# Performance work log

Measured on AMD Instinct MI355X. Metric: run time of the kernel, lower is better.

Reference implementation:

```python
import jax, jax.numpy as jnp
import numpy as np

B, C1, C2, H, W = 16, 64, 64, 160, 160
K, KS, HID = 4, 3, 16  # K kernels, 3x3, hidden = max(int(64/16),16)=16
EPS = 1e-5


def setup_inputs() -> dict:
    key = jax.random.key(0)
    ks = jax.random.split(key, 8)
    fan_out = KS * KS * C2
    return {
        "x": jax.random.normal(ks[0], (B, C1, H, W), jnp.float32),
        # K candidate conv kernels and biases
        "Wk": jax.random.normal(ks[1], (K, C2, C1, KS, KS), jnp.float32) * np.sqrt(2.0 / fan_out),
        "bk": jnp.zeros((K, C2), jnp.float32),
        # attention trunk: 1x1 conv C1->HID (no bias), BN, ReLU
        "Wfc": jax.random.normal(ks[2], (HID, C1), jnp.float32) * 0.1,
        "gamma_h": jnp.ones((HID,), jnp.float32),
        "beta_h": jnp.zeros((HID,), jnp.float32),
        # four attention heads
        "Wf": jax.random.normal(ks[3], (C2, HID), jnp.float32) * 0.1,
        "bf": jnp.zeros((C2,), jnp.float32),
        "Ws": jax.random.normal(ks[4], (KS * KS, HID), jnp.float32) * 0.1,
        "bs": jnp.zeros((KS * KS,), jnp.float32),
        "Wc": jax.random.normal(ks[5], (C1, HID), jnp.float32) * 0.1,
        "bc": jnp.zeros((C1,), jnp.float32),
        "Ww": jax.random.normal(ks[6], (K, HID), jnp.float32) * 0.1,
        "bw": jnp.zeros((K,), jnp.float32),
        # outer BatchNorm2d params
        "gamma_o": jnp.ones((C2,), jnp.float32),
        "beta_o": jnp.zeros((C2,), jnp.float32),
    }


def reference(x, Wk, bk, Wfc, gamma_h, beta_h, Wf, bf, Ws, bs, Wc, bc, Ww, bw, gamma_o, beta_o):
    # ---- per-sample attention over K kernels ----
    ctx = x.mean(axis=(2, 3))                      # (B, C1)  global avg pool
    h = ctx @ Wfc.T                                # (B, HID) 1x1 conv == linear
    mu = h.mean(axis=0)
    var = h.var(axis=0)                            # biased, as torch BN training
    h = (h - mu) / jnp.sqrt(var + EPS) * gamma_h + beta_h
    h = jax.nn.relu(h)
    attn_f = jax.nn.sigmoid(h @ Wf.T + bf)         # (B, C2)
    attn_s = jax.nn.sigmoid(h @ Ws.T + bs).reshape(B, KS, KS)
    attn_c = jax.nn.sigmoid(h @ Wc.T + bc)         # (B, C1)
    attn_w = jax.nn.softmax(h @ Ww.T + bw, axis=-1)  # (B, K)

    # attn: (B, K, C2, C1, KS, KS) via broadcasting
    attn = (attn_w[:, :, None, None, None, None]
            * attn_f[:, None, :, None, None, None]
            * attn_c[:, None, None, :, None, None]
            * attn_s[:, None, None, None, :, :])
    weight = jnp.sum(attn * Wk[None], axis=1)      # (B, C2, C1, KS, KS)
    bias = attn_w @ bk                             # (B, C2)

    # ---- batched conv as grouped conv with groups=B ----
    out = jax.lax.conv_general_dilated(
        x.reshape(1, B * C1, H, W),
        weight.reshape(B * C2, C1, KS, KS),
        window_strides=(1, 1), padding=((1, 1), (1, 1)),
        dimension_numbers=('NCHW', 'OIHW', 'NCHW'),
        feature_group_count=B)                     # (1, B*C2, H, W)
    out = out.reshape(B, C2, H, W) + bias[:, :, None, None]

    # ---- outer BatchNorm2d (training stats) + SiLU ----
    mu_o = out.mean(axis=(0, 2, 3))
    var_o = out.var(axis=(0, 2, 3))
    out = (out - mu_o[None, :, None, None]) / jnp.sqrt(var_o + EPS)[None, :, None, None]
    out = out * gamma_o[None, :, None, None] + beta_o[None, :, None, None]
    return out * jax.nn.sigmoid(out)               # SiLU
```

## Files before the change

kernel.cpp:

```cpp
#include <hip/hip_runtime.h>
#include <math.h>

#define BB 16
#define C1 64
#define C2 64
#define HH 160
#define WW 160
#define KK 4
#define HID 16
#define EPS 1e-5f
#define HWSZ (HH*WW)
#define NPB (BB*HWSZ)

#define WS_AF    1024
#define WS_AC    2048
#define WS_AS    3072
#define WS_AW    3216
#define WS_BIAS  3280
#define WS_STATS 4432
#define NSLOT    32
#define WS_PART  8704
#define WS_WEFF  53760
#define WS_XBF   348672
#define WS_OBF   13455872
#define WS_NEED_BYTES 106252288ULL

typedef __attribute__((ext_vector_type(8)))  short bf16x8;
typedef __attribute__((ext_vector_type(16))) float f32x16;

__device__ __forceinline__ unsigned short f2bf(float f) {
    unsigned int u = __float_as_uint(f);
    unsigned int r = (u + 0x7FFFu + ((u >> 16) & 1u)) >> 16;
    return (unsigned short)r;
}

__device__ __forceinline__ void gload16(const void* g, void* l) {
    __builtin_amdgcn_global_load_lds(
        (const __attribute__((address_space(1))) unsigned int*)g,
        (__attribute__((address_space(3))) unsigned int*)l, 16, 0, 0);
}

__global__ __launch_bounds__(256) void xprep_kernel(const float* __restrict__ x,
                                                    float* __restrict__ ws) {
    __shared__ float lds[10240];
    int bcc = blockIdx.y;
    int rg = blockIdx.x;
    int t = threadIdx.x;

    const float* src = x + (size_t)bcc * 16 * HWSZ + (size_t)rg * 4 * WW;
    float4* l4 = (float4*)lds;
    #pragma unroll
    for (int i = 0; i < 10; ++i) {
        int g = i * 256 + t;
        int ch = g / 160, rem = g - ch * 160;
        l4[g] = *(const float4*)(src + (size_t)ch * HWSZ + rem * 4);
    }
    __syncthreads();

    {
        int ch = t >> 4, j = t & 15;
        float s = 0.f;
        #pragma unroll
        for (int m = 0; m < 40; ++m) s += lds[ch * 640 + j + 16 * m];
        #pragma unroll
        for (int o = 8; o > 0; o >>= 1) s += __shfl_down(s, o, 16);
        if (j == 0) ws[WS_PART + ((size_t)bcc * 40 + rg) * 16 + ch] = s;
    }

    uint4* dst = (uint4*)(ws + WS_XBF) + ((size_t)bcc * 160 + rg * 4) * 320;
    #pragma unroll
    for (int i = 0; i < 5; ++i) {
        int u = i * 256 + t;
        int row = u / 320, rem = u - row * 320;
        int col = rem >> 1, p = rem & 1;
        int h = p ^ ((col >> 2) & 1) ^ 1;
        union { uint4 q; unsigned short us[8]; } pk;
        #pragma unroll
        for (int k = 0; k < 8; ++k)
            pk.us[k] = f2bf(lds[(h * 8 + k) * 640 + row * 160 + col]);
        dst[u] = pk.q;
    }
}

__global__ void attn_kernel(float* __restrict__ ws,
    const float* __restrict__ Wfc, const float* __restrict__ gh, const float* __restrict__ bh,
    const float* __restrict__ Wf,  const float* __restrict__ bf,
    const float* __restrict__ Wsm, const float* __restrict__ bs,
    const float* __restrict__ Wc,  const float* __restrict__ bc,
    const float* __restrict__ Ww,  const float* __restrict__ bw,
    const float* __restrict__ bk) {
    __shared__ float ctxs[16][64];
    __shared__ float hs[16][16];
    __shared__ float aw[16][4];
    int t = threadIdx.x;

    #pragma unroll
    for (int q = 0; q < 4; ++q) {
        int idx = t * 4 + q;
        int b = idx >> 6, c1 = idx & 63;
        const float* pp = ws + WS_PART + ((size_t)(b * 4 + (c1 >> 4)) * 40) * 16 + (c1 & 15);
        float s = 0.f;
        #pragma unroll
        for (int rg = 0; rg < 40; ++rg) s += pp[rg * 16];
        ctxs[b][c1] = s * (1.0f / (float)HWSZ);
    }
    __syncthreads();
    {
        int b = t >> 4, j = t & 15;
        const float* wr = Wfc + j * 64;
        float s = 0.f;
        #pragma unroll
        for (int c = 0; c < 64; c++) s += ctxs[b][c] * wr[c];
        hs[b][j] = s;
    }
    __syncthreads();
    if (t < 16) {
        int j = t;
        float mu = 0.f;
        #pragma unroll
        for (int b = 0; b < 16; b++) mu += hs[b][j];
        mu *= (1.f / 16.f);
        float vr = 0.f;
        #pragma unroll
        for (int b = 0; b < 16; b++) { float d = hs[b][j] - mu; vr += d * d; }
        vr *= (1.f / 16.f);
        float sc = gh[j] * rsqrtf(vr + EPS);
        float sh = bh[j] - mu * sc;
        #pragma unroll
        for (int b = 0; b < 16; b++) {
            float v = hs[b][j] * sc + sh;
            hs[b][j] = v > 0.f ? v : 0.f;
        }
    }
    __syncthreads();
    if (t < 16) {
        int b = t;
        float l[4]; float mx = -1e30f;
        #pragma unroll
        for (int k = 0; k < 4; k++) {
            float s = bw[k];
            #pragma unroll
            for (int j = 0; j < 16; j++) s += hs[b][j] * Ww[k * 16 + j];
            l[k] = s; mx = fmaxf(mx, s);
        }
        float den = 0.f;
        #pragma unroll
        for (int k = 0; k < 4; k++) { l[k] = expf(l[k] - mx); den += l[k]; }
        float r = 1.f / den;
        #pragma unroll
        for (int k = 0; k < 4; k++) { float v = l[k] * r; aw[b][k] = v; ws[WS_AW + b * 4 + k] = v; }
    }
    #pragma unroll
    for (int q = 0; q < 4; q++) {
        int idx = t * 4 + q;
        int b = idx >> 6, c2 = idx & 63;
        float sf = bf[c2], sc2 = bc[c2];
        #pragma unroll
        for (int j = 0; j < 16; j++) {
            float hv = hs[b][j];
            sf  += hv * Wf[c2 * 16 + j];
            sc2 += hv * Wc[c2 * 16 + j];
        }
        ws[WS_AF + idx] = 1.f / (1.f + expf(-sf));
        ws[WS_AC + idx] = 1.f / (1.f + expf(-sc2));
    }
    if (t < 144) {
        int b = t / 9, uv = t % 9;
        float s = bs[uv];
        #pragma unroll
        for (int j = 0; j < 16; j++) s += hs[b][j] * Wsm[uv * 16 + j];
        ws[WS_AS + t] = 1.f / (1.f + expf(-s));
    }
    __syncthreads();
    #pragma unroll
    for (int q = 0; q < 4; q++) {
        int idx = t * 4 + q;
        int b = idx >> 6, c2 = idx & 63;
        float s = 0.f;
        #pragma unroll
        for (int k = 0; k < 4; k++) s += aw[b][k] * bk[k * 64 + c2];
        ws[WS_BIAS + idx] = s;
    }
    for (int i = t; i < NSLOT * 128; i += 256) ws[WS_STATS + i] = 0.f;
}

__global__ void wprep_kernel(const float* __restrict__ Wk, float* __restrict__ ws) {
    int b = blockIdx.y;
    int tid = blockIdx.x * 256 + threadIdx.x;
    int h = tid & 1;
    int c2 = (tid >> 1) & 63;
    int g = tid >> 7;
    int uv = g % 9;
    int chunk = g / 9;
    const float* awp = ws + WS_AW + b * 4;
    float aw0 = awp[0], aw1 = awp[1], aw2 = awp[2], aw3 = awp[3];
    float af = ws[WS_AF + b * 64 + c2];
    float as_ = ws[WS_AS + b * 9 + uv];
    union { uint4 q; unsigned short u[8]; } pk;
    #pragma unroll
    for (int j = 0; j < 8; ++j) {
        int c1 = chunk * 16 + h * 8 + j;
        const float* wp = Wk + (size_t)(c2 * 64 + c1) * 9 + uv;
        float s = aw0 * wp[0] + aw1 * wp[64 * 64 * 9] + aw2 * wp[2 * 64 * 64 * 9] + aw3 * wp[3 * 64 * 64 * 9];
        float w = s * af * ws[WS_AC + b * 64 + c1] * as_;
        pk.u[j] = f2bf(w);
    }
    int unit = ((chunk * 9 + uv) * 64 + c2) * 2 + (h ^ ((c2 >> 2) & 1));
    ((uint4*)(ws + WS_WEFF))[(size_t)b * 4608 + unit] = pk.q;
}

template<int OBF>
__launch_bounds__(256, 3)
__global__ void conv_kernel(const float* __restrict__ wsf, float* __restrict__ out) {
    __shared__ uint4 xs[4 * 162 * 2];
    __shared__ uint4 wsh[1152];
    __shared__ float bsh[64];
    __shared__ float sst[128];

    int id = blockIdx.x;
    int b = id & 15;
    int bx = id >> 4;
    int y0 = bx * 2;
    int t = threadIdx.x;
    int wv = t >> 6;
    int lane = t & 63;
    int l31 = lane & 31;
    int l5 = lane >> 5;
    int c2h = wv & 1;
    int rw = wv >> 1;

    if (t < 64) bsh[t] = wsf[WS_BIAS + b * 64 + t];
    if (t >= 64 && t < 192) sst[t - 64] = 0.f;
    if (t >= 192 && t < 208) {
        int q = t - 192;
        int r = q >> 2, side = (q >> 1) & 1, p = q & 1;
        xs[(r * 162 + side * 161) * 2 + p] = make_uint4(0, 0, 0, 0);
    }
    int rbad = (bx == 0) ? 0 : (bx == 79 ? 3 : -1);
    if (rbad >= 0) {
        for (int i = t; i < 320; i += 256)
            xs[(rbad * 162 + 1) * 2 + i] = make_uint4(0, 0, 0, 0);
    }

    const uint4* weff = (const uint4*)(wsf + WS_WEFF) + (size_t)b * 4608;
    const uint4* xbf  = (const uint4*)(wsf + WS_XBF);

    f32x16 acc[5];
    #pragma unroll
    for (int j = 0; j < 5; ++j)
        #pragma unroll
        for (int r = 0; r < 16; ++r) acc[j][r] = 0.f;

    int c2 = c2h * 32 + l31;
    int aswz = (l31 >> 2) & 1;
    for (int cc = 0; cc < 4; ++cc) {
        __syncthreads();
        for (int i = wv; i < 18; i += 4)
            gload16(weff + (size_t)cc * 1152 + i * 64 + lane, (char*)wsh + i * 1024);
        for (int i = wv; i < 20; i += 4) {
            int r = i / 5, seg = i % 5;
            int gy = y0 - 1 + r;
            if (gy >= 0 && gy < HH)
                gload16(xbf + (((size_t)b * 4 + cc) * 160 + gy) * 320 + seg * 64 + lane,
                        (char*)xs + ((r * 162 + 1) * 2 + seg * 64) * 16);
        }
        __syncthreads();

        #pragma unroll
        for (int uv = 0; uv < 9; ++uv) {
            bf16x8 a = *(bf16x8*)&wsh[(uv * 64 + c2) * 2 + (l5 ^ aswz)];
            int xr = rw + uv / 3;
            int v = uv % 3;
            #pragma unroll
            for (int j = 0; j < 5; ++j) {
                int col = j * 32 + l31 + v;
                bf16x8 bb = *(bf16x8*)&xs[(xr * 162 + col) * 2 + (l5 ^ (((col + 3) >> 2) & 1))];
                acc[j] = __builtin_amdgcn_mfma_f32_32x32x16_bf16(a, bb, acc[j], 0, 0, 0);
            }
        }
    }

    float* outb = out + (size_t)b * C2 * HWSZ + (size_t)(y0 + rw) * WW;
    unsigned short* obfb = (unsigned short*)((float*)wsf + WS_OBF)
                         + (size_t)b * C2 * HWSZ + (size_t)(y0 + rw) * WW;
    int cb = c2h * 32 + 4 * l5;
    float sr[16], qr[16];
    #pragma unroll
    for (int r = 0; r < 16; ++r) {
        int c2r = cb + (r & 3) + 8 * (r >> 2);
        float bias = bsh[c2r];
        float s = 0.f, q = 0.f;
        #pragma unroll
        for (int j = 0; j < 5; ++j) {
            float v = acc[j][r] + bias;
            if (OBF) obfb[(size_t)c2r * HWSZ + j * 32 + l31] = f2bf(v);
            else     outb[(size_t)c2r * HWSZ + j * 32 + l31] = v;
            s += v;
            q = fmaf(v, v, q);
        }
        sr[r] = s; qr[r] = q;
    }
    #pragma unroll
    for (int k = 0; k < 4; ++k) {
        int m = 1 << k, n = 8 >> k;
        #pragma unroll
        for (int i = 0; i < 8; ++i) {
            if (i < n) {
                float ks = (l31 & m) ? sr[i + n] : sr[i];
                float ss = (l31 & m) ? sr[i] : sr[i + n];
                sr[i] = ks + __shfl_xor(ss, m, 64);
                float kq = (l31 & m) ? qr[i + n] : qr[i];
                float sq = (l31 & m) ? qr[i] : qr[i + n];
                qr[i] = kq + __shfl_xor(sq, m, 64);
            }
        }
    }
    sr[0] += __shfl_xor(sr[0], 16, 64);
    qr[0] += __shfl_xor(qr[0], 16, 64);
    if (l31 < 16) {
        int rf = ((l31 & 1) << 3) | ((l31 & 2) << 1) | ((l31 & 4) >> 1) | ((l31 & 8) >> 3);
        int c2r = cb + (rf & 3) + 8 * (rf >> 2);
        atomicAdd(&sst[c2r], sr[0]);
        atomicAdd(&sst[64 + c2r], qr[0]);
    }
    __syncthreads();
    if (t < 128) {
        int slot = id & (NSLOT - 1);
        atomicAdd((float*)wsf + WS_STATS + slot * 128 + t, sst[t]);
    }
}

template<int OBF>
__global__ void bnact_kernel(float* __restrict__ out, const float* __restrict__ ws,
                             const float* __restrict__ go, const float* __restrict__ bo) {
    __shared__ float sc[64], sh[64];
    if (threadIdx.x < 64) {
        int c = threadIdx.x;
        float s = 0.f, q = 0.f;
        #pragma unroll
        for (int sl = 0; sl < NSLOT; sl++) {
            s += ws[WS_STATS + sl * 128 + c];
            q += ws[WS_STATS + sl * 128 + 64 + c];
        }
        float mu  = s * (1.0f / (float)NPB);
        float var = q * (1.0f / (float)NPB) - mu * mu;
        float scale = go[c] * rsqrtf(var + EPS);
        sc[c] = scale;
        sh[c] = bo[c] - mu * scale;
    }
    __syncthreads();
    const unsigned short* obf = (const unsigned short*)(ws + WS_OBF);
    const int n4 = BB * C2 * HWSZ / 4;
    for (int i = blockIdx.x * blockDim.x + threadIdx.x; i < n4; i += gridDim.x * blockDim.x) {
        float4 v;
        if (OBF) {
            ushort4 u = ((const ushort4*)obf)[i];
            v.x = __uint_as_float((unsigned)u.x << 16);
            v.y = __uint_as_float((unsigned)u.y << 16);
            v.z = __uint_as_float((unsigned)u.z << 16);
            v.w = __uint_as_float((unsigned)u.w << 16);
        } else {
            v = ((float4*)out)[i];
        }
        int c = ((i * 4) / HWSZ) & 63;
        float s = sc[c], h = sh[c];
        v.x = v.x * s + h; v.y = v.y * s + h; v.z = v.z * s + h; v.w = v.w * s + h;
        v.x = v.x / (1.f + __expf(-v.x));
        v.y = v.y / (1.f + __expf(-v.y));
        v.z = v.z / (1.f + __expf(-v.z));
        v.w = v.w / (1.f + __expf(-v.w));
        ((float4*)out)[i] = v;
    }
}

extern "C" void kernel_launch(void* const* d_in, const int* in_sizes, int n_in,
                              void* d_out, int out_size, void* d_ws, size_t ws_size,
                              hipStream_t stream) {
    const float* x   = (const float*)d_in[0];
    const float* Wk  = (const float*)d_in[1];
    const float* bk  = (const float*)d_in[2];
    const float* Wfc = (const float*)d_in[3];
    const float* gh  = (const float*)d_in[4];
    const float* bh  = (const float*)d_in[5];
    const float* Wf  = (const float*)d_in[6];
    const float* bf  = (const float*)d_in[7];
    const float* Wsm = (const float*)d_in[8];
    const float* bs  = (const float*)d_in[9];
    const float* Wc  = (const float*)d_in[10];
    const float* bc  = (const float*)d_in[11];
    const float* Ww  = (const float*)d_in[12];
    const float* bw  = (const float*)d_in[13];
    const float* go  = (const float*)d_in[14];
    const float* bo  = (const float*)d_in[15];
    float* out = (float*)d_out;
    float* ws  = (float*)d_ws;

    bool use_obf = (ws_size >= WS_NEED_BYTES);

    xprep_kernel<<<dim3(40, 64), dim3(256), 0, stream>>>(x, ws);
    attn_kernel<<<dim3(1), dim3(256), 0, stream>>>(ws, Wfc, gh, bh, Wf, bf, Wsm, bs, Wc, bc, Ww, bw, bk);
    wprep_kernel<<<dim3(18, 16), dim3(256), 0, stream>>>(Wk, ws);
    if (use_obf) {
        conv_kernel<1><<<dim3(1280), dim3(256), 0, stream>>>(ws, out);
        bnact_kernel<1><<<dim3(2048), dim3(256), 0, stream>>>(out, ws, go, bo);
    } else {
        conv_kernel<0><<<dim3(1280), dim3(256), 0, stream>>>(ws, out);
        bnact_kernel<0><<<dim3(2048), dim3(256), 0, stream>>>(out, ws, go, bo);
    }
}
```

Before: 129.8 us.

## Split conv into single-wave blocks with register-held weights and direct stats atomics

Each conv block shrinks from four waves to one wave covering a single output row and half the output channels, launched as four times as many blocks. Effective weights now go straight from global memory into registers instead of shared memory, and the per-block LDS stat reduction is replaced by direct global atomics. This drops the block-wide barriers and cuts shared memory per block. In exchange, each input row is loaded by more blocks (a 3-row halo per output row instead of per two rows), weight reads are repeated per block, and contention on the global stats atomics goes up.

```diff
diff --git a/kernel.cpp b/kernel.cpp
--- a/kernel.cpp
+++ b/kernel.cpp
@@ -210,40 +210,31 @@
 }
 
 template<int OBF>
-__launch_bounds__(256, 3)
+__launch_bounds__(64, 2)
 __global__ void conv_kernel(const float* __restrict__ wsf, float* __restrict__ out) {
-    __shared__ uint4 xs[4 * 162 * 2];
-    __shared__ uint4 wsh[1152];
-    __shared__ float bsh[64];
-    __shared__ float sst[128];
+    __shared__ uint4 xs[3][324];
 
     int id = blockIdx.x;
     int b = id & 15;
-    int bx = id >> 4;
-    int y0 = bx * 2;
-    int t = threadIdx.x;
-    int wv = t >> 6;
-    int lane = t & 63;
+    int rem = id >> 4;
+    int y = rem >> 1;
+    int c2h = rem & 1;
+    int lane = threadIdx.x;
     int l31 = lane & 31;
     int l5 = lane >> 5;
-    int c2h = wv & 1;
-    int rw = wv >> 1;
-
-    if (t < 64) bsh[t] = wsf[WS_BIAS + b * 64 + t];
-    if (t >= 64 && t < 192) sst[t - 64] = 0.f;
-    if (t >= 192 && t < 208) {
-        int q = t - 192;
-        int r = q >> 2, side = (q >> 1) & 1, p = q & 1;
-        xs[(r * 162 + side * 161) * 2 + p] = make_uint4(0, 0, 0, 0);
-    }
-    int rbad = (bx == 0) ? 0 : (bx == 79 ? 3 : -1);
-    if (rbad >= 0) {
-        for (int i = t; i < 320; i += 256)
-            xs[(rbad * 162 + 1) * 2 + i] = make_uint4(0, 0, 0, 0);
-    }
-
-    const uint4* weff = (const uint4*)(wsf + WS_WEFF) + (size_t)b * 4608;
-    const uint4* xbf  = (const uint4*)(wsf + WS_XBF);
+
+    if (lane < 12) {
+        int r = lane >> 2, q = lane & 3;
+        xs[r][(q >> 1) * 322 + (q & 1)] = make_uint4(0, 0, 0, 0);
+    }
+    if (y == 0)   for (int i = lane; i < 324; i += 64) xs[0][i] = make_uint4(0, 0, 0, 0);
+    if (y == 159) for (int i = lane; i < 324; i += 64) xs[2][i] = make_uint4(0, 0, 0, 0);
+
+    const char*  weffb = (const char*)(wsf + WS_WEFF) + (size_t)b * 73728;
+    const uint4* xbf   = (const uint4*)(wsf + WS_XBF);
+
+    int c2 = c2h * 32 + l31;
+    int a_off = (c2 * 2 + (l5 ^ ((c2 >> 2) & 1))) * 16;
 
     f32x16 acc[5];
     #pragma unroll
@@ -251,44 +242,50 @@
         #pragma unroll
         for (int r = 0; r < 16; ++r) acc[j][r] = 0.f;
 
-    int c2 = c2h * 32 + l31;
-    int aswz = (l31 >> 2) & 1;
     for (int cc = 0; cc < 4; ++cc) {
-        __syncthreads();
-        for (int i = wv; i < 18; i += 4)
-            gload16(weff + (size_t)cc * 1152 + i * 64 + lane, (char*)wsh + i * 1024);
-        for (int i = wv; i < 20; i += 4) {
-            int r = i / 5, seg = i % 5;
-            int gy = y0 - 1 + r;
-            if (gy >= 0 && gy < HH)
-                gload16(xbf + (((size_t)b * 4 + cc) * 160 + gy) * 320 + seg * 64 + lane,
-                        (char*)xs + ((r * 162 + 1) * 2 + seg * 64) * 16);
-        }
-        __syncthreads();
+        const uint4* xcc = xbf + ((size_t)(b * 4 + cc) * 160) * 320;
+        #pragma unroll
+        for (int u = 0; u < 3; ++u) {
+            int gy = y - 1 + u;
+            if (gy >= 0 && gy < HH) {
+                const uint4* src = xcc + gy * 320 + lane;
+                #pragma unroll
+                for (int seg = 0; seg < 5; ++seg)
+                    gload16(src + seg * 64, (char*)&xs[u][2] + seg * 1024);
+            }
+        }
+        const char* wrow = weffb + cc * 18432;
+        bf16x8 av[9];
+        #pragma unroll
+        for (int uv = 0; uv < 9; ++uv)
+            av[uv] = *(const bf16x8*)(wrow + uv * 2048 + a_off);
+
+        asm volatile("s_waitcnt vmcnt(0) lgkmcnt(0)" ::: "memory");
+        __builtin_amdgcn_sched_barrier(0);
 
         #pragma unroll
         for (int uv = 0; uv < 9; ++uv) {
-            bf16x8 a = *(bf16x8*)&wsh[(uv * 64 + c2) * 2 + (l5 ^ aswz)];
-            int xr = rw + uv / 3;
-            int v = uv % 3;
+            int u = uv / 3, v = uv % 3;
             #pragma unroll
             for (int j = 0; j < 5; ++j) {
                 int col = j * 32 + l31 + v;
-                bf16x8 bb = *(bf16x8*)&xs[(xr * 162 + col) * 2 + (l5 ^ (((col + 3) >> 2) & 1))];
-                acc[j] = __builtin_amdgcn_mfma_f32_32x32x16_bf16(a, bb, acc[j], 0, 0, 0);
+                bf16x8 bb = *(bf16x8*)&xs[u][col * 2 + (l5 ^ (((col + 3) >> 2) & 1))];
+                acc[j] = __builtin_amdgcn_mfma_f32_32x32x16_bf16(av[uv], bb, acc[j], 0, 0, 0);
             }
         }
-    }
-
-    float* outb = out + (size_t)b * C2 * HWSZ + (size_t)(y0 + rw) * WW;
+        asm volatile("s_waitcnt lgkmcnt(0)" ::: "memory");
+        __builtin_amdgcn_sched_barrier(0);
+    }
+
+    float* outb = out + (size_t)b * C2 * HWSZ + (size_t)y * WW;
     unsigned short* obfb = (unsigned short*)((float*)wsf + WS_OBF)
-                         + (size_t)b * C2 * HWSZ + (size_t)(y0 + rw) * WW;
+                         + (size_t)b * C2 * HWSZ + (size_t)y * WW;
     int cb = c2h * 32 + 4 * l5;
     float sr[16], qr[16];
     #pragma unroll
     for (int r = 0; r < 16; ++r) {
         int c2r = cb + (r & 3) + 8 * (r >> 2);
-        float bias = bsh[c2r];
+        float bias = wsf[WS_BIAS + b * 64 + c2r];
         float s = 0.f, q = 0.f;
         #pragma unroll
         for (int j = 0; j < 5; ++j) {
@@ -320,13 +317,9 @@
     if (l31 < 16) {
         int rf = ((l31 & 1) << 3) | ((l31 & 2) << 1) | ((l31 & 4) >> 1) | ((l31 & 8) >> 3);
         int c2r = cb + (rf & 3) + 8 * (rf >> 2);
-        atomicAdd(&sst[c2r], sr[0]);
-        atomicAdd(&sst[64 + c2r], qr[0]);
-    }
-    __syncthreads();
-    if (t < 128) {
-        int slot = id & (NSLOT - 1);
-        atomicAdd((float*)wsf + WS_STATS + slot * 128 + t, sst[t]);
+        float* st = (float*)wsf + WS_STATS + (size_t)(id & (NSLOT - 1)) * 128;
+        atomicAdd(&st[c2r], sr[0]);
+        atomicAdd(&st[64 + c2r], qr[0]);
     }
 }
 
@@ -401,10 +394,10 @@
     attn_kernel<<<dim3(1), dim3(256), 0, stream>>>(ws, Wfc, gh, bh, Wf, bf, Wsm, bs, Wc, bc, Ww, bw, bk);
     wprep_kernel<<<dim3(18, 16), dim3(256), 0, stream>>>(Wk, ws);
     if (use_obf) {
-        conv_kernel<1><<<dim3(1280), dim3(256), 0, stream>>>(ws, out);
+        conv_kernel<1><<<dim3(5120), dim3(64), 0, stream>>>(ws, out);
         bnact_kernel<1><<<dim3(2048), dim3(256), 0, stream>>>(out, ws, go, bo);
     } else {
-        conv_kernel<0><<<dim3(1280), dim3(256), 0, stream>>>(ws, out);
+        conv_kernel<0><<<dim3(5120), dim3(64), 0, stream>>>(ws, out);
         bnact_kernel<0><<<dim3(2048), dim3(256), 0, stream>>>(out, ws, go, bo);
     }
 }
```

New measurement: 129.8 us. No clear change (+0.1%).
